# Kernel tuning notes

Measured on AMD Instinct MI355X. Metric: run time of the kernel, lower is better.

Reference implementation:

```python
import jax, jax.numpy as jnp
import numpy as np

DIM = 1  # quantization axis (channels)


def setup_inputs() -> dict:
    key = jax.random.key(0)
    kx, kc = jax.random.split(key)
    x = jax.random.normal(kx, (32, 256, 32, 32), dtype=jnp.float32)
    # nn.init.normal_(weight, 0, 1.1)
    codebook = 1.1 * jax.random.normal(kc, (8192, 256), dtype=jnp.float32)
    return {"x": x, "codebook": codebook}


def reference(x, codebook):
    # move quantization dim to last: [B, C, H, W] -> [B, W, H, C]
    xt = jnp.swapaxes(x, -1, DIM)
    flat = xt.reshape(-1, xt.shape[-1])  # [N, D]
    # squared distances ||f - c||^2 = ||f||^2 - 2 f.c + ||c||^2  -> [N, K]
    d2 = (jnp.sum(flat * flat, axis=1, keepdims=True)
          - 2.0 * (flat @ codebook.T)
          + jnp.sum(codebook * codebook, axis=1))
    idx = jnp.argmin(d2, axis=1)                      # [N]
    codes = codebook[idx].reshape(xt.shape)           # nearest-code gather
    indices = idx.reshape(xt.shape[:-1])
    # transpose back to original layout
    codes = jnp.swapaxes(codes, -1, DIM)              # [B, C, H, W]
    indices = jnp.swapaxes(indices, -1, DIM)          # [B, H, W]
    return codes, indices
```

## Files before the change

kernel.cpp:

```cpp
#include <hip/hip_runtime.h>
#include <math.h>


typedef _Float16 v8h __attribute__((ext_vector_type(8)));
typedef float f32x16 __attribute__((ext_vector_type(16)));
typedef unsigned int u32;

#define MFMA16 __builtin_amdgcn_mfma_f32_32x32x16_f16

__device__ __forceinline__ void gll16(const _Float16* g, _Float16* l) {
  __builtin_amdgcn_global_load_lds(
      (const __attribute__((address_space(1))) void*)(const void*)g,
      (__attribute__((address_space(3))) void*)(void*)l, 16, 0, 0);
}

__global__ __launch_bounds__(256) void cnorm_k(const float4* __restrict__ cb4,
                                               float* __restrict__ cn) {
  int lane = threadIdx.x & 63;
  int row = (blockIdx.x << 2) + (threadIdx.x >> 6);
  float4 v = cb4[(size_t)row * 64 + lane];
  float s = v.x * v.x + v.y * v.y + v.z * v.z + v.w * v.w;
#pragma unroll
  for (int off = 32; off > 0; off >>= 1) s += __shfl_xor(s, off, 64);
  if (lane == 0) cn[row] = s;
}

__global__ __launch_bounds__(256) void split_cb(const float4* __restrict__ cb4,
                                                _Float16* __restrict__ W) {
  const int j = threadIdx.x & 31;
  const int ks = j >> 1, hi = j & 1;
  const int r = (blockIdx.x << 3) + (threadIdx.x >> 5);
  const float4* src = cb4 + (size_t)r * 64 + (ks << 2) + (hi << 1);
  float4 v0 = src[0], v1 = src[1];
  float t[8] = {v0.x, v0.y, v0.z, v0.w, v1.x, v1.y, v1.z, v1.w};
  v8h hv, mv;
#pragma unroll
  for (int i = 0; i < 8; ++i) {
    float vs = t[i] * 8192.f;
    _Float16 h = (_Float16)vs;
    _Float16 m = (_Float16)(vs - (float)h);
    hv[i] = h; mv[i] = m;
  }
  const int wv = (r >> 6) & 7, c64 = r & 63;
  _Float16* base = W + ((size_t)((r >> 9) << 4) + ks) * 16384 + (wv << 11);
  *(v8h*)(base + (hi << 9) + (c64 << 3)) = hv;
  *(v8h*)(base + 1024 + (hi << 9) + (c64 << 3)) = mv;
}

#define STEP_BODY(P, Q, DO_CNV)                                              \
  asm volatile("s_waitcnt lgkmcnt(0)" ::: "memory");  \
  if (DO_CNV) {             \
    cnv0 = cn[(ct << 9) + (w << 6) + col];                                   \
    cnv1 = cn[(ct << 9) + (w << 6) + 32 + col];                              \
  }                                                                          \
  if (st < 254) {                                                            \
    const _Float16* gsrc = W + ((size_t)(st + 2) << 14) + chunk + (lane << 3); \
    gll16(gsrc,        &Bsh[P][chunk]);                                      \
    gll16(gsrc + 512,  &Bsh[P][chunk + 512]);                                \
    gll16(gsrc + 1024, &Bsh[P][chunk + 1024]);                               \
    gll16(gsrc + 1536, &Bsh[P][chunk + 1536]);                               \
    asm volatile("s_waitcnt vmcnt(4)" ::: "memory");  \
  } else {                                                                   \
    asm volatile("s_waitcnt vmcnt(0)" ::: "memory");                         \
  }                                                                          \
  if (st < 255) {                                                            \
    const int ksq = (st + 1) & 15;                                           \
    Af[Q][0] = *(const v8h*)&F2L[ksq][0][0][hi][col][0];                     \
    Af[Q][1] = *(const v8h*)&F2L[ksq][0][1][hi][col][0];                     \
    Af[Q][2] = *(const v8h*)&F2L[ksq][1][0][hi][col][0];                     \
    Af[Q][3] = *(const v8h*)&F2L[ksq][1][1][hi][col][0];                     \
    const _Float16* Bb = &Bsh[Q][0];                                         \
    Bf[Q][0] = *(const v8h*)&Bb[rb0];                                        \
    Bf[Q][1] = *(const v8h*)&Bb[rb0 + 256];                                  \
    Bf[Q][2] = *(const v8h*)&Bb[rb0 + 1024];                                 \
    Bf[Q][3] = *(const v8h*)&Bb[rb0 + 1280];                                 \
  }                                                                          \
  a00 = MFMA16(Af[P][0], Bf[P][0], a00, 0, 0, 0);                            \
  a01 = MFMA16(Af[P][0], Bf[P][1], a01, 0, 0, 0);                            \
  a10 = MFMA16(Af[P][1], Bf[P][0], a10, 0, 0, 0);                            \
  a11 = MFMA16(Af[P][1], Bf[P][1], a11, 0, 0, 0);                            \
  a00 = MFMA16(Af[P][0], Bf[P][2], a00, 0, 0, 0);                            \
  a01 = MFMA16(Af[P][0], Bf[P][3], a01, 0, 0, 0);                            \
  a10 = MFMA16(Af[P][1], Bf[P][2], a10, 0, 0, 0);                            \
  a11 = MFMA16(Af[P][1], Bf[P][3], a11, 0, 0, 0);                            \
  a00 = MFMA16(Af[P][2], Bf[P][0], a00, 0, 0, 0);                            \
  a01 = MFMA16(Af[P][2], Bf[P][1], a01, 0, 0, 0);                            \
  a10 = MFMA16(Af[P][3], Bf[P][0], a10, 0, 0, 0);                            \
  a11 = MFMA16(Af[P][3], Bf[P][1], a11, 0, 0, 0);

__global__ void __launch_bounds__(512, 1) vq_fast(const float* __restrict__ x,
                                                  const float4* __restrict__ cb4,
                                                  const float* __restrict__ cn,
                                                  const _Float16* __restrict__ W,
                                                  float* __restrict__ out) {
  __shared__ __align__(16) _Float16 F2L[16][2][2][2][32][8];
  __shared__ __align__(16) _Float16 Bsh[2][16384];
  __shared__ float fnP[64][8];
  __shared__ float fnS[64];
  __shared__ float wredS[8][64];
  __shared__ u32  wredC[8][64];
  __shared__ u32  finS[64];

  const int tid = threadIdx.x;
  const int lane = tid & 63;
  const int w = tid >> 6;
  const int col = lane & 31;
  const int hi = lane >> 5;
  const int b = blockIdx.x >> 4;
  const int h0 = (blockIdx.x & 15) << 1;

  const int chunk = w << 11;
  const int rb0 = chunk + (hi << 9) + (col << 3);

  {
    const _Float16* s0 = W + chunk + (lane << 3);
#pragma unroll
    for (int k = 0; k < 4; ++k) gll16(s0 + (k << 9), &Bsh[0][chunk + (k << 9)]);
#pragma unroll
    for (int k = 0; k < 4; ++k) gll16(s0 + 16384 + (k << 9), &Bsh[1][chunk + (k << 9)]);
  }

  {
    const float* xb = x + ((size_t)b << 18) + (h0 << 5);
    const int Mb = lane >> 5, cl = lane & 31;
    float s = 0.f;
#pragma unroll
    for (int j = 0; j < 2; ++j) {
      const int ks = (w << 1) + j;
#pragma unroll
      for (int fh = 0; fh < 2; ++fh) {
        v8h hv, mv;
#pragma unroll
        for (int i = 0; i < 8; ++i) {
          const int c = (ks << 4) + (fh << 3) + i;
          float v = xb[(size_t)c * 1024 + lane];
          s += v * v;
          float vs = v * 8192.f;
          _Float16 h = (_Float16)vs;
          _Float16 m = (_Float16)(vs - (float)h);
          hv[i] = h; mv[i] = m;
        }
        *(v8h*)&F2L[ks][0][Mb][fh][cl][0] = hv;
        *(v8h*)&F2L[ks][1][Mb][fh][cl][0] = mv;
      }
    }
    fnP[lane][w] = s;
  }
  __syncthreads();
  if (tid < 64) {
    float t = 0.f;
#pragma unroll
    for (int j = 0; j < 8; ++j) t += fnP[tid][j];
    fnS[tid] = t;
  }
  __syncthreads();

  float fnr[32];
#pragma unroll
  for (int sl = 0; sl < 32; ++sl) {
    const int row = ((sl >> 4) << 5) + (sl & 3) + (((sl >> 2) & 3) << 3) + (hi << 2);
    fnr[sl] = fnS[row];
  }

  v8h Af[2][4], Bf[2][4];
  {
    Af[0][0] = *(const v8h*)&F2L[0][0][0][hi][col][0];
    Af[0][1] = *(const v8h*)&F2L[0][0][1][hi][col][0];
    Af[0][2] = *(const v8h*)&F2L[0][1][0][hi][col][0];
    Af[0][3] = *(const v8h*)&F2L[0][1][1][hi][col][0];
    const _Float16* Bb = &Bsh[0][0];
    Bf[0][0] = *(const v8h*)&Bb[rb0];
    Bf[0][1] = *(const v8h*)&Bb[rb0 + 256];
    Bf[0][2] = *(const v8h*)&Bb[rb0 + 1024];
    Bf[0][3] = *(const v8h*)&Bb[rb0 + 1280];
  }

  f32x16 a00, a01, a10, a11;
#pragma unroll
  for (int r = 0; r < 16; ++r) { a00[r] = 0.f; a01[r] = 0.f; a10[r] = 0.f; a11[r] = 0.f; }
  float mn[32];
#pragma unroll
  for (int sl = 0; sl < 32; ++sl) mn[sl] = INFINITY;
  u32 idp[8] = {0, 0, 0, 0, 0, 0, 0, 0};

#pragma unroll 1
  for (int ct = 0; ct < 16; ++ct) {
    float cnv0, cnv1;
#pragma unroll
    for (int kk = 0; kk < 8; ++kk) {
      {
        const int st = (ct << 4) + (kk << 1);
        STEP_BODY(0, 1, (kk == 0))
      }
      {
        const int st = (ct << 4) + (kk << 1) + 1;
        STEP_BODY(1, 0, false)
      }
    }
#pragma unroll
    for (int sl = 0; sl < 32; ++sl) {
      const int Mb = sl >> 4, reg = sl & 15;
      const float base = fnr[sl];
      const u32 sh = (u32)((sl & 3) << 3);
      {
        const float d = (Mb == 0) ? a00[reg] : a10[reg];
        float s = (base + (-0x1p-25f) * d) + cnv0;
        const bool better = s < mn[sl];
        const u32 curv = idp[sl >> 2];
        const u32 upd = (curv & ~(255u << sh)) | (((u32)(ct << 1)) << sh);
        idp[sl >> 2] = better ? upd : curv;
        mn[sl] = better ? s : mn[sl];
      }
      {
        const float d = (Mb == 0) ? a01[reg] : a11[reg];
        float s = (base + (-0x1p-25f) * d) + cnv1;
        const bool better = s < mn[sl];
        const u32 curv = idp[sl >> 2];
        const u32 upd = (curv & ~(255u << sh)) | (((u32)((ct << 1) | 1)) << sh);
        idp[sl >> 2] = better ? upd : curv;
        mn[sl] = better ? s : mn[sl];
      }
    }
#pragma unroll
    for (int r = 0; r < 16; ++r) { a00[r] = 0.f; a01[r] = 0.f; a10[r] = 0.f; a11[r] = 0.f; }
  }

#pragma unroll
  for (int sl = 0; sl < 32; ++sl) {
    float v = mn[sl];
    const u32 byte = (idp[sl >> 2] >> ((sl & 3) << 3)) & 255u;
    u32 code = ((byte >> 1) << 9) + ((u32)w << 6) + ((byte & 1) << 5) + (u32)col;
#pragma unroll
    for (int off = 1; off < 32; off <<= 1) {
      float v2 = __shfl_xor(v, off, 64);
      u32 c2 = (u32)__shfl_xor((int)code, off, 64);
      if (v2 < v || (v2 == v && c2 < code)) { v = v2; code = c2; }
    }
    if (col == 0) {
      const int row = ((sl >> 4) << 5) + (sl & 3) + (((sl >> 2) & 3) << 3) + (hi << 2);
      wredS[w][row] = v; wredC[w][row] = code;
    }
  }
  __syncthreads();
  if (tid < 64) {
    float bv = wredS[0][tid]; u32 bc = wredC[0][tid];
#pragma unroll
    for (int j = 1; j < 8; ++j) {
      float vv = wredS[j][tid]; u32 cc = wredC[j][tid];
      if (vv < bv || (vv == bv && cc < bc)) { bv = vv; bc = cc; }
    }
    finS[tid] = bc;
    out[(size_t)8388608 + ((size_t)b << 10) + (h0 << 5) + tid] = (float)bc;
  }
  __syncthreads();

  {
    const int pt = tid & 63, cg = tid >> 6;
    const u32 code = finS[pt];
    const float4* cbr = cb4 + ((size_t)code << 6);
    const size_t obase = ((size_t)b << 18) + (h0 << 5) + pt;
#pragma unroll
    for (int cc = 0; cc < 8; ++cc) {
      const int c4 = (cc << 3) + cg;
      float4 vv = cbr[c4];
      out[obase + (size_t)((c4 << 2) + 0) * 1024] = vv.x;
      out[obase + (size_t)((c4 << 2) + 1) * 1024] = vv.y;
      out[obase + (size_t)((c4 << 2) + 2) * 1024] = vv.z;
      out[obase + (size_t)((c4 << 2) + 3) * 1024] = vv.w;
    }
  }
}

__global__ void __launch_bounds__(512, 2) vq_fb(const float* __restrict__ x,
                                                const float4* __restrict__ cb4,
                                                const float* __restrict__ cn,
                                                float* __restrict__ out) {
  __shared__ __align__(16) _Float16 F2[2][64][264];
  __shared__ __align__(16) _Float16 Bsh[512][72];
  __shared__ float fnP[64][8];
  __shared__ float fnS[64];
  __shared__ float wredS[8][64];
  __shared__ u32  wredC[8][64];
  __shared__ u32  finS[64];

  const int tid = threadIdx.x;
  const int lane = tid & 63;
  const int w = tid >> 6;
  const int col = lane & 31;
  const int hi = lane >> 5;
  const int b = blockIdx.x >> 4;
  const int h0 = (blockIdx.x & 15) << 1;

  float4 rg[8];
  {
    const float4* src = cb4 + ((size_t)tid << 6);
#pragma unroll
    for (int j = 0; j < 8; ++j) rg[j] = src[j];
  }
  {
    const float* xb = x + ((size_t)b << 18) + (h0 << 5);
    float s = 0.f;
#pragma unroll
    for (int j = 0; j < 4; ++j) {
      v8h hv, mv;
#pragma unroll
      for (int i = 0; i < 8; ++i) {
        const int c = (w << 5) + (j << 3) + i;
        float v = xb[(size_t)c * 1024 + lane];
        s += v * v;
        float vs = v * 8192.f;
        _Float16 h = (_Float16)vs;
        _Float16 m = (_Float16)(vs - (float)h);
        hv[i] = h; mv[i] = m;
      }
      *(v8h*)&F2[0][lane][(w << 5) + (j << 3)] = hv;
      *(v8h*)&F2[1][lane][(w << 5) + (j << 3)] = mv;
    }
    fnP[lane][w] = s;
  }
  __syncthreads();
  if (tid < 64) {
    float t = 0.f;
#pragma unroll
    for (int j = 0; j < 8; ++j) t += fnP[tid][j];
    fnS[tid] = t;
  }
  {
#pragma unroll
    for (int j = 0; j < 4; ++j) {
      float t0[8] = {rg[2*j].x, rg[2*j].y, rg[2*j].z, rg[2*j].w,
                     rg[2*j+1].x, rg[2*j+1].y, rg[2*j+1].z, rg[2*j+1].w};
      v8h hv, mv;
#pragma unroll
      for (int i = 0; i < 8; ++i) {
        float vs = t0[i] * 8192.f;
        _Float16 h = (_Float16)vs;
        _Float16 m = (_Float16)(vs - (float)h);
        hv[i] = h; mv[i] = m;
      }
      *(v8h*)&Bsh[tid][(j << 3)] = hv;
      *(v8h*)&Bsh[tid][32 + (j << 3)] = mv;
    }
  }
  __syncthreads();

  float fnr[32];
#pragma unroll
  for (int sl = 0; sl < 32; ++sl) {
    const int row = ((sl >> 4) << 5) + (sl & 3) + (((sl >> 2) & 3) << 3) + (hi << 2);
    fnr[sl] = fnS[row];
  }

  f32x16 acc[2][2];
#pragma unroll
  for (int r = 0; r < 16; ++r) {
    acc[0][0][r] = 0.f; acc[0][1][r] = 0.f; acc[1][0][r] = 0.f; acc[1][1][r] = 0.f;
  }
  float mn[32];
#pragma unroll
  for (int sl = 0; sl < 32; ++sl) mn[sl] = INFINITY;
  u32 idp[8] = {0, 0, 0, 0, 0, 0, 0, 0};
  float cnv0 = 0.f, cnv1 = 0.f;

  for (int st = 0; st < 128; ++st) {
    const int ks = st & 7, ct = st >> 3;
    if (st < 127) {
      const int tn = st + 1;
      const float4* src = cb4 + ((size_t)((((tn >> 3) << 9) + tid)) << 6) + ((tn & 7) << 3);
#pragma unroll
      for (int j = 0; j < 8; ++j) rg[j] = src[j];
    }
    if (ks == 0) {
      cnv0 = cn[(ct << 9) + (w << 6) + col];
      cnv1 = cn[(ct << 9) + (w << 6) + 32 + col];
    }
    const int kb = ks << 5;
#pragma unroll
    for (int kh = 0; kh < 2; ++kh) {
      const int ko = kb + (kh << 4) + (hi << 3);
      const v8h ah0 = *(const v8h*)&F2[0][col][ko];
      const v8h ah1 = *(const v8h*)&F2[0][32 + col][ko];
      const v8h am0 = *(const v8h*)&F2[1][col][ko];
      const v8h am1 = *(const v8h*)&F2[1][32 + col][ko];
      const int bo = (kh << 4) + (hi << 3);
      const v8h bh0 = *(const v8h*)&Bsh[(w << 6) + col][bo];
      const v8h bh1 = *(const v8h*)&Bsh[(w << 6) + 32 + col][bo];
      const v8h bm0 = *(const v8h*)&Bsh[(w << 6) + col][32 + bo];
      const v8h bm1 = *(const v8h*)&Bsh[(w << 6) + 32 + col][32 + bo];
      acc[0][0] = MFMA16(ah0, bh0, acc[0][0], 0, 0, 0);
      acc[0][0] = MFMA16(ah0, bm0, acc[0][0], 0, 0, 0);
      acc[0][0] = MFMA16(am0, bh0, acc[0][0], 0, 0, 0);
      acc[0][1] = MFMA16(ah0, bh1, acc[0][1], 0, 0, 0);
      acc[0][1] = MFMA16(ah0, bm1, acc[0][1], 0, 0, 0);
      acc[0][1] = MFMA16(am0, bh1, acc[0][1], 0, 0, 0);
      acc[1][0] = MFMA16(ah1, bh0, acc[1][0], 0, 0, 0);
      acc[1][0] = MFMA16(ah1, bm0, acc[1][0], 0, 0, 0);
      acc[1][0] = MFMA16(am1, bh0, acc[1][0], 0, 0, 0);
      acc[1][1] = MFMA16(ah1, bh1, acc[1][1], 0, 0, 0);
      acc[1][1] = MFMA16(ah1, bm1, acc[1][1], 0, 0, 0);
      acc[1][1] = MFMA16(am1, bh1, acc[1][1], 0, 0, 0);
    }
    if (ks == 7) {
#pragma unroll
      for (int sl = 0; sl < 32; ++sl) {
        const int Mb = sl >> 4, reg = sl & 15;
        const float base = fnr[sl];
        const u32 sh = (u32)((sl & 3) << 3);
        {
          float s = (base + (-0x1p-25f) * acc[Mb][0][reg]) + cnv0;
          const bool better = s < mn[sl];
          const u32 curv = idp[sl >> 2];
          const u32 upd = (curv & ~(255u << sh)) | (((u32)(ct << 1)) << sh);
          idp[sl >> 2] = better ? upd : curv;
          mn[sl] = better ? s : mn[sl];
        }
        {
          float s = (base + (-0x1p-25f) * acc[Mb][1][reg]) + cnv1;
          const bool better = s < mn[sl];
          const u32 curv = idp[sl >> 2];
          const u32 upd = (curv & ~(255u << sh)) | (((u32)((ct << 1) | 1)) << sh);
          idp[sl >> 2] = better ? upd : curv;
          mn[sl] = better ? s : mn[sl];
        }
      }
#pragma unroll
      for (int r = 0; r < 16; ++r) {
        acc[0][0][r] = 0.f; acc[0][1][r] = 0.f; acc[1][0][r] = 0.f; acc[1][1][r] = 0.f;
      }
    }
    v8h cr[8];
    if (st < 127) {
#pragma unroll
      for (int j = 0; j < 4; ++j) {
        float t0[8] = {rg[2*j].x, rg[2*j].y, rg[2*j].z, rg[2*j].w,
                       rg[2*j+1].x, rg[2*j+1].y, rg[2*j+1].z, rg[2*j+1].w};
#pragma unroll
        for (int i = 0; i < 8; ++i) {
          float vs = t0[i] * 8192.f;
          _Float16 h = (_Float16)vs;
          _Float16 m = (_Float16)(vs - (float)h);
          cr[j][i] = h; cr[4 + j][i] = m;
        }
      }
    }
    __syncthreads();
    if (st < 127) {
#pragma unroll
      for (int j = 0; j < 4; ++j) {
        *(v8h*)&Bsh[tid][(j << 3)] = cr[j];
        *(v8h*)&Bsh[tid][32 + (j << 3)] = cr[4 + j];
      }
    }
    __syncthreads();
  }

#pragma unroll
  for (int sl = 0; sl < 32; ++sl) {
    float v = mn[sl];
    const u32 byte = (idp[sl >> 2] >> ((sl & 3) << 3)) & 255u;
    u32 code = ((byte >> 1) << 9) + ((u32)w << 6) + ((byte & 1) << 5) + (u32)col;
#pragma unroll
    for (int off = 1; off < 32; off <<= 1) {
      float v2 = __shfl_xor(v, off, 64);
      u32 c2 = (u32)__shfl_xor((int)code, off, 64);
      if (v2 < v || (v2 == v && c2 < code)) { v = v2; code = c2; }
    }
    if (col == 0) {
      const int row = ((sl >> 4) << 5) + (sl & 3) + (((sl >> 2) & 3) << 3) + (hi << 2);
      wredS[w][row] = v; wredC[w][row] = code;
    }
  }
  __syncthreads();
  if (tid < 64) {
    float bv = wredS[0][tid]; u32 bc = wredC[0][tid];
#pragma unroll
    for (int j = 1; j < 8; ++j) {
      float vv = wredS[j][tid]; u32 cc = wredC[j][tid];
      if (vv < bv || (vv == bv && cc < bc)) { bv = vv; bc = cc; }
    }
    finS[tid] = bc;
    out[(size_t)8388608 + ((size_t)b << 10) + (h0 << 5) + tid] = (float)bc;
  }
  __syncthreads();
  {
    const int pt = tid & 63, cg = tid >> 6;
    const u32 code = finS[pt];
    const float4* cbr = cb4 + ((size_t)code << 6);
    const size_t obase = ((size_t)b << 18) + (h0 << 5) + pt;
#pragma unroll
    for (int cc = 0; cc < 8; ++cc) {
      const int c4 = (cc << 3) + cg;
      float4 vv = cbr[c4];
      out[obase + (size_t)((c4 << 2) + 0) * 1024] = vv.x;
      out[obase + (size_t)((c4 << 2) + 1) * 1024] = vv.y;
      out[obase + (size_t)((c4 << 2) + 2) * 1024] = vv.z;
      out[obase + (size_t)((c4 << 2) + 3) * 1024] = vv.w;
    }
  }
}

extern "C" void kernel_launch(void* const* d_in, const int* in_sizes, int n_in,
                              void* d_out, int out_size, void* d_ws, size_t ws_size,
                              hipStream_t stream) {
  const float* x = (const float*)d_in[0];
  const float* cb = (const float*)d_in[1];
  float* out = (float*)d_out;
  float* cnorm = (float*)d_ws;

  cnorm_k<<<2048, 256, 0, stream>>>((const float4*)cb, cnorm);
  if (ws_size >= (size_t)32768 + (size_t)8388608) {
    _Float16* W = (_Float16*)((char*)d_ws + 32768);
    split_cb<<<1024, 256, 0, stream>>>((const float4*)cb, W);
    vq_fast<<<512, 512, 0, stream>>>(x, (const float4*)cb, cnorm, W, out);
  } else {
    vq_fb<<<512, 512, 0, stream>>>(x, (const float4*)cb, cnorm, out);
  }
}
```

Measured before the change: 449.1 us.

## Load codebook B fragments directly from global into registers, drop LDS staging

Removes the LDS double buffer for the split-fp16 codebook and its global_load_lds prefetch and waitcnt handshakes. Each wave now loads its B fragments straight from global memory into registers two steps ahead, issuing the loads after the MFMAs. Launch bounds rise to two blocks per CU, made possible by the freed LDS. The risk is exposed global-load latency and more register pressure under the tighter occupancy bound, plus no LDS reuse of B data.

```diff
diff --git a/kernel.cpp b/kernel.cpp
--- a/kernel.cpp
+++ b/kernel.cpp
@@ -7,12 +7,6 @@
 typedef unsigned int u32;
 
 #define MFMA16 __builtin_amdgcn_mfma_f32_32x32x16_f16
-
-__device__ __forceinline__ void gll16(const _Float16* g, _Float16* l) {
-  __builtin_amdgcn_global_load_lds(
-      (const __attribute__((address_space(1))) void*)(const void*)g,
-      (__attribute__((address_space(3))) void*)(void*)l, 16, 0, 0);
-}
 
 __global__ __launch_bounds__(256) void cnorm_k(const float4* __restrict__ cb4,
                                                float* __restrict__ cn) {
@@ -48,20 +42,9 @@
 }
 
 #define STEP_BODY(P, Q, DO_CNV)                                              \
-  asm volatile("s_waitcnt lgkmcnt(0)" ::: "memory");  \
-  if (DO_CNV) {             \
+  if (DO_CNV) {                                                              \
     cnv0 = cn[(ct << 9) + (w << 6) + col];                                   \
     cnv1 = cn[(ct << 9) + (w << 6) + 32 + col];                              \
-  }                                                                          \
-  if (st < 254) {                                                            \
-    const _Float16* gsrc = W + ((size_t)(st + 2) << 14) + chunk + (lane << 3); \
-    gll16(gsrc,        &Bsh[P][chunk]);                                      \
-    gll16(gsrc + 512,  &Bsh[P][chunk + 512]);                                \
-    gll16(gsrc + 1024, &Bsh[P][chunk + 1024]);                               \
-    gll16(gsrc + 1536, &Bsh[P][chunk + 1536]);                               \
-    asm volatile("s_waitcnt vmcnt(4)" ::: "memory");  \
-  } else {                                                                   \
-    asm volatile("s_waitcnt vmcnt(0)" ::: "memory");                         \
   }                                                                          \
   if (st < 255) {                                                            \
     const int ksq = (st + 1) & 15;                                           \
@@ -69,11 +52,6 @@
     Af[Q][1] = *(const v8h*)&F2L[ksq][0][1][hi][col][0];                     \
     Af[Q][2] = *(const v8h*)&F2L[ksq][1][0][hi][col][0];                     \
     Af[Q][3] = *(const v8h*)&F2L[ksq][1][1][hi][col][0];                     \
-    const _Float16* Bb = &Bsh[Q][0];                                         \
-    Bf[Q][0] = *(const v8h*)&Bb[rb0];                                        \
-    Bf[Q][1] = *(const v8h*)&Bb[rb0 + 256];                                  \
-    Bf[Q][2] = *(const v8h*)&Bb[rb0 + 1024];                                 \
-    Bf[Q][3] = *(const v8h*)&Bb[rb0 + 1280];                                 \
   }                                                                          \
   a00 = MFMA16(Af[P][0], Bf[P][0], a00, 0, 0, 0);                            \
   a01 = MFMA16(Af[P][0], Bf[P][1], a01, 0, 0, 0);                            \
@@ -86,15 +64,21 @@
   a00 = MFMA16(Af[P][2], Bf[P][0], a00, 0, 0, 0);                            \
   a01 = MFMA16(Af[P][2], Bf[P][1], a01, 0, 0, 0);                            \
   a10 = MFMA16(Af[P][3], Bf[P][0], a10, 0, 0, 0);                            \
-  a11 = MFMA16(Af[P][3], Bf[P][1], a11, 0, 0, 0);
-
-__global__ void __launch_bounds__(512, 1) vq_fast(const float* __restrict__ x,
+  a11 = MFMA16(Af[P][3], Bf[P][1], a11, 0, 0, 0);                            \
+  if (st < 254) {                                                            \
+    const v8h* bsrc = (const v8h*)(Wb + (((size_t)(st + 2)) << 15) + boff);  \
+    Bf[P][0] = bsrc[0];                                                      \
+    Bf[P][1] = bsrc[32];                                        \
+    Bf[P][2] = bsrc[128];                                       \
+    Bf[P][3] = bsrc[160];                                       \
+  }
+
+__global__ void __launch_bounds__(512, 2) vq_fast(const float* __restrict__ x,
                                                   const float4* __restrict__ cb4,
                                                   const float* __restrict__ cn,
                                                   const _Float16* __restrict__ W,
                                                   float* __restrict__ out) {
   __shared__ __align__(16) _Float16 F2L[16][2][2][2][32][8];
-  __shared__ __align__(16) _Float16 Bsh[2][16384];
   __shared__ float fnP[64][8];
   __shared__ float fnS[64];
   __shared__ float wredS[8][64];
@@ -109,15 +93,15 @@
   const int b = blockIdx.x >> 4;
   const int h0 = (blockIdx.x & 15) << 1;
 
-  const int chunk = w << 11;
-  const int rb0 = chunk + (hi << 9) + (col << 3);
-
-  {
-    const _Float16* s0 = W + chunk + (lane << 3);
-#pragma unroll
-    for (int k = 0; k < 4; ++k) gll16(s0 + (k << 9), &Bsh[0][chunk + (k << 9)]);
-#pragma unroll
-    for (int k = 0; k < 4; ++k) gll16(s0 + 16384 + (k << 9), &Bsh[1][chunk + (k << 9)]);
+  const char* Wb = (const char*)W;
+  const size_t boff = (size_t)(((w << 11) + (hi << 9) + (col << 3)) << 1);
+
+  v8h Af[2][4], Bf[2][4];
+  {
+    const v8h* b0 = (const v8h*)(Wb + boff);
+    Bf[0][0] = b0[0];  Bf[0][1] = b0[32];  Bf[0][2] = b0[128];  Bf[0][3] = b0[160];
+    const v8h* b1 = (const v8h*)(Wb + 32768 + boff);
+    Bf[1][0] = b1[0];  Bf[1][1] = b1[32];  Bf[1][2] = b1[128];  Bf[1][3] = b1[160];
   }
 
   {
@@ -162,17 +146,11 @@
     fnr[sl] = fnS[row];
   }
 
-  v8h Af[2][4], Bf[2][4];
   {
     Af[0][0] = *(const v8h*)&F2L[0][0][0][hi][col][0];
     Af[0][1] = *(const v8h*)&F2L[0][0][1][hi][col][0];
     Af[0][2] = *(const v8h*)&F2L[0][1][0][hi][col][0];
     Af[0][3] = *(const v8h*)&F2L[0][1][1][hi][col][0];
-    const _Float16* Bb = &Bsh[0][0];
-    Bf[0][0] = *(const v8h*)&Bb[rb0];
-    Bf[0][1] = *(const v8h*)&Bb[rb0 + 256];
-    Bf[0][2] = *(const v8h*)&Bb[rb0 + 1024];
-    Bf[0][3] = *(const v8h*)&Bb[rb0 + 1280];
   }
 
   f32x16 a00, a01, a10, a11;
```

Measured after the change: 799.8 us. 78.1% more time.
